# Kernel optimization log

Hardware: AMD Instinct MI355X
Metric: run time of the kernel (lower is better)

The kernel has to match this reference:

```python
import jax, jax.numpy as jnp
import numpy as np
from jax import lax

WIN = 11
SIGMA = 1.5
C1 = 0.01 ** 2
C2 = 0.03 ** 2


def _gauss_window(c):
    x = np.arange(WIN) - WIN // 2
    g = np.exp(-(x ** 2) / (2.0 * SIGMA ** 2))
    g = g / g.sum()
    w2d = np.outer(g, g).astype(np.float32)  # [11,11]
    return jnp.asarray(np.broadcast_to(w2d, (c, 1, WIN, WIN)).copy())


def _dwconv(x, kernel, groups):
    # x: [B,C,H,W], kernel: [C,1,kh,kw] depthwise, stride 1, SAME padding
    return lax.conv_general_dilated(
        x, kernel, window_strides=(1, 1), padding='SAME',
        dimension_numbers=('NCHW', 'OIHW', 'NCHW'),
        feature_group_count=groups)


_SOBEL_X = jnp.asarray(np.array([[-1, 0, 1], [-2, 0, 2], [-1, 0, 1]], np.float32))
_SOBEL_Y = jnp.asarray(np.array([[1, 2, 1], [0, 0, 0], [-1, -2, -1]], np.float32))


def _sobel_xy(x):
    # x: [B,3,H,W] -> depthwise 3x3 sobel on each channel (same as per-channel conv2d)
    c = x.shape[1]
    kx = jnp.broadcast_to(_SOBEL_X, (c, 1, 3, 3))
    ky = jnp.broadcast_to(_SOBEL_Y, (c, 1, 3, 3))
    return _dwconv(x, kx, c), _dwconv(x, ky, c)


def _rgb2ycrcb(im):
    R, G, B = im[:, 0:1], im[:, 1:2], im[:, 2:3]
    Y = 0.299 * R + 0.587 * G + 0.114 * B
    Cr = (R - Y) * 0.713 + 0.5
    Cb = (B - Y) * 0.564 + 0.5
    return Y, Cr, Cb


def _ssim(img1, img2, channel):
    w = _gauss_window(channel)
    mu1 = _dwconv(img1, w, channel)
    mu2 = _dwconv(img2, w, channel)
    mu1_sq = mu1 * mu1
    mu2_sq = mu2 * mu2
    mu12 = mu1 * mu2
    s1 = _dwconv(img1 * img1, w, channel) - mu1_sq
    s2 = _dwconv(img2 * img2, w, channel) - mu2_sq
    s12 = _dwconv(img1 * img2, w, channel) - mu12
    ssim_map = ((2 * mu12 + C1) * (2 * s12 + C2)) / ((mu1_sq + mu2_sq + C1) * (s1 + s2 + C2))
    return ssim_map.mean()


def _l1(a, b):
    return jnp.mean(jnp.abs(a - b))


def setup_inputs() -> dict:
    key = jax.random.key(0)
    k1, k2, k3 = jax.random.split(key, 3)
    shp = (16, 3, 512, 512)
    return {
        'input_vis': jax.random.uniform(k1, shp, jnp.float32),
        'input_ir': jax.random.uniform(k2, shp, jnp.float32),
        'fuse': jax.random.uniform(k3, shp, jnp.float32),
    }


def reference(input_vis, input_ir, fuse):
    # color components
    _, Cr_F, Cb_F = _rgb2ycrcb(fuse)
    _, Cr_V, Cb_V = _rgb2ycrcb(input_vis)
    Y_ir = input_ir[:, 0:1]

    # sobel gradients (depthwise over 3 channels == per-channel conv + cat)
    Fgx, Fgy = _sobel_xy(fuse)
    Vgx, Vgy = _sobel_xy(input_vis)
    Igx, Igy = _sobel_xy(input_ir)
    joint_gx = jnp.maximum(Vgx, Igx)
    joint_gy = jnp.maximum(Vgy, Igy)
    joint_int = jnp.maximum(input_vis, input_ir)

    con_loss = _l1(fuse, joint_int)
    gradient_loss = 0.5 * _l1(Fgx, joint_gx) + 0.5 * _l1(Fgy, joint_gy)
    color_loss = _l1(Cb_F, Cb_V) + _l1(Cr_F, Cr_V)

    # SSIM: rgb-vs-fused (3ch) and ir-Y vs gray(fused) (1ch)
    ssim_rgb = _ssim(input_vis, fuse, 3)
    gray_fused = (0.2989 * fuse[:, 0:1] + 0.587 * fuse[:, 1:2] + 0.114 * fuse[:, 2:3])
    ssim_ir = _ssim(Y_ir, gray_fused, 1)
    ssim_loss = 1.0 - (ssim_rgb + ssim_ir) / 2.0

    return 0.5 * con_loss + 0.2 * gradient_loss + 1.0 * color_loss + 0.1 * ssim_loss
```

## Files before the change

kernel.cpp:

```cpp
#include <hip/hip_runtime.h>

#define IMG_H 512
#define IMG_W 512
#define CH_STRIDE (IMG_H*IMG_W)
#define IMG_STRIDE (3*CH_STRIDE)

using f4 = __attribute__((ext_vector_type(4))) float;
using h2 = __attribute__((ext_vector_type(2))) _Float16;
using h4 = __attribute__((ext_vector_type(4))) _Float16;
using h8 = __attribute__((ext_vector_type(8))) _Float16;

#define NSLOT 64
#define SLOT_F 32

__global__ __launch_bounds__(256) void k_zero(float* __restrict__ acc) {
  int i = threadIdx.x;
  *(f4*)&acc[i*8]     = f4{0,0,0,0};
  *(f4*)&acc[i*8 + 4] = f4{0,0,0,0};
}

__device__ __forceinline__ float block_sum(float v, float* red) {
  #pragma unroll
  for (int o = 32; o > 0; o >>= 1) v += __shfl_down(v, o, 64);
  __syncthreads();
  if ((threadIdx.x & 63) == 0) red[threadIdx.x >> 6] = v;
  __syncthreads();
  return red[0] + red[1] + red[2] + red[3];
}

__device__ __forceinline__ h8 splat8(_Float16 v) { return h8{v,v,v,v,v,v,v,v}; }

#define R1W 68
#define R1N (18*R1W)

#define SXW 80
#define SXH 42
#define HB8 264
#define SSIM_SX_B (SXH*SXW*2)
#define SSIM_HB_B (SXH*HB8*2)
#define SMEM_BYTES (2*SSIM_SX_B + SSIM_HB_B)

__global__ __launch_bounds__(256, 4) void k_main(
    const float* __restrict__ vis, const float* __restrict__ ir,
    const float* __restrict__ fuse, float* __restrict__ acc)
{
  __shared__ __align__(16) char smem[SMEM_BYTES];
  __shared__ float red[4];
  const int tid = threadIdx.x;
  const int bid = blockIdx.x;
  float* aslot = acc + (bid & (NSLOT-1))*SLOT_F;

  if (bid < 8192) {
    const int z = bid >> 7;
    const int n = z >> 2, pair = z & 3;
    const int x0 = (bid & 7)*64;
    const int y0 = ((bid >> 3) & 15)*32;
    _Float16* sx = (_Float16*)smem;
    _Float16* sy = (_Float16*)(smem + SSIM_SX_B);
    _Float16* hb = (_Float16*)(smem + 2*SSIM_SX_B);

    _Float16 gh[11];
    h2 gh2[11];
    {
      const float gu[6] = {0.00386592014f, 0.02856550078f, 0.13533528324f,
                           0.41111229050f, 0.80073740292f, 1.0f};
      float g[11], gs = 0.f;
      #pragma unroll
      for (int i = 0; i < 11; ++i) { g[i] = gu[i < 6 ? i : 10 - i]; gs += g[i]; }
      #pragma unroll
      for (int i = 0; i < 11; ++i) {
        g[i] /= gs;
        gh[i] = (_Float16)g[i];
        gh2[i] = h2{gh[i], gh[i]};
      }
    }

    if (pair < 3) {
      const float* xb = vis  + (n*3 + pair)*CH_STRIDE;
      const float* yb = fuse + (n*3 + pair)*CH_STRIDE;
      for (int i = tid; i < SXH*20; i += 256) {
        int row = i / 20, k = i - row*20;
        int gy = y0 - 5 + row, gx = x0 - 8 + 4*k;
        f4 xv = {0,0,0,0}, yv = {0,0,0,0};
        if ((unsigned)gy < IMG_H && (unsigned)gx < IMG_W) {
          int off = gy*IMG_W + gx;
          xv = *(const f4*)&xb[off];
          yv = *(const f4*)&yb[off];
        }
        int ib = row*SXW + 4*k;
        *(h4*)&sx[ib] = h4{(_Float16)xv.x,(_Float16)xv.y,(_Float16)xv.z,(_Float16)xv.w};
        *(h4*)&sy[ib] = h4{(_Float16)yv.x,(_Float16)yv.y,(_Float16)yv.z,(_Float16)yv.w};
      }
    } else {
      const float* xb = ir   + n*IMG_STRIDE;
      const float* fb = fuse + n*IMG_STRIDE;
      for (int i = tid; i < SXH*20; i += 256) {
        int row = i / 20, k = i - row*20;
        int gy = y0 - 5 + row, gx = x0 - 8 + 4*k;
        f4 xv = {0,0,0,0}, yv = {0,0,0,0};
        if ((unsigned)gy < IMG_H && (unsigned)gx < IMG_W) {
          int off = gy*IMG_W + gx;
          xv = *(const f4*)&xb[off];
          f4 rr = *(const f4*)&fb[off];
          f4 gg = *(const f4*)&fb[off + CH_STRIDE];
          f4 bb = *(const f4*)&fb[off + 2*CH_STRIDE];
          #pragma unroll
          for (int j = 0; j < 4; ++j)
            yv[j] = 0.2989f*rr[j] + 0.587f*gg[j] + 0.114f*bb[j];
        }
        int ib = row*SXW + 4*k;
        *(h4*)&sx[ib] = h4{(_Float16)xv.x,(_Float16)xv.y,(_Float16)xv.z,(_Float16)xv.w};
        *(h4*)&sy[ib] = h4{(_Float16)yv.x,(_Float16)yv.y,(_Float16)yv.z,(_Float16)yv.w};
      }
    }
    __syncthreads();

    for (int t = tid; t < SXH*8; t += 256) {
      int row = t >> 3, p0 = (t & 7)*4;
      int base = row*SXW + p0*2;
      h8 xa0 = *(const h8*)&sx[base];
      h8 xa1 = *(const h8*)&sx[base+8];
      h8 xa2 = *(const h8*)&sx[base+16];
      h8 yb0 = *(const h8*)&sy[base];
      h8 yb1 = *(const h8*)&sy[base+8];
      h8 yb2 = *(const h8*)&sy[base+16];
      _Float16 wa[21], wb[21];
      #pragma unroll
      for (int u = 0; u < 21; ++u) {
        wa[u] = (u < 8 ? xa0[u] : (u < 16 ? xa1[u-8] : xa2[u-16]));
        wb[u] = (u < 8 ? yb0[u] : (u < 16 ? yb1[u-8] : yb2[u-16]));
      }
      h2 pa[14], pb[14], pp[14], pq[14];
      #pragma unroll
      for (int u = 0; u < 14; ++u) {
        pa[u] = h2{wa[u+3], wa[u+7]};
        pb[u] = h2{wb[u+3], wb[u+7]};
        pp[u] = pa[u]*pa[u] + pb[u]*pb[u];
        pq[u] = pa[u]*pb[u];
      }
      h2 cA[4], cB[4], cP[4], cQ[4];
      #pragma unroll
      for (int j = 0; j < 4; ++j) { cA[j]=h2{0,0}; cB[j]=h2{0,0}; cP[j]=h2{0,0}; cQ[j]=h2{0,0}; }
      #pragma unroll
      for (int k = 0; k < 11; ++k) {
        h2 gk = gh2[k];
        #pragma unroll
        for (int j = 0; j < 4; ++j) {
          cA[j] += gk * pa[k+j];
          cB[j] += gk * pb[k+j];
          cP[j] += gk * pp[k+j];
          cQ[j] += gk * pq[k+j];
        }
      }
      #pragma unroll
      for (int p = 0; p < 4; ++p) {
        int j0 = 2*p, j1 = 2*p + 1;
        _Float16 a0 = (j0 < 4) ? cA[j0][0] : cA[j0-4][1];
        _Float16 b0 = (j0 < 4) ? cB[j0][0] : cB[j0-4][1];
        _Float16 P0 = (j0 < 4) ? cP[j0][0] : cP[j0-4][1];
        _Float16 q0 = (j0 < 4) ? cQ[j0][0] : cQ[j0-4][1];
        _Float16 a1 = (j1 < 4) ? cA[j1][0] : cA[j1-4][1];
        _Float16 b1 = (j1 < 4) ? cB[j1][0] : cB[j1-4][1];
        _Float16 P1 = (j1 < 4) ? cP[j1][0] : cP[j1-4][1];
        _Float16 q1 = (j1 < 4) ? cQ[j1][0] : cQ[j1-4][1];
        *(h8*)&hb[row*HB8 + (p0 + p)*8] = h8{a0,b0,P0,q0,a1,b1,P1,q1};
      }
    }
    __syncthreads();

    const int xp = tid & 31;
    const int ybase = (tid >> 5)*4;
    h8 vacc[4];
    #pragma unroll
    for (int m = 0; m < 4; ++m) vacc[m] = splat8((_Float16)0.f);
    #pragma unroll
    for (int r = 0; r < 14; ++r) {
      h8 rv = *(const h8*)&hb[(ybase + r)*HB8 + xp*8];
      #pragma unroll
      for (int m = 0; m < 4; ++m) {
        int k = r - m;
        if (k >= 0 && k < 11) vacc[m] += splat8(gh[k]) * rv;
      }
    }

    float ss = 0.f;
    #pragma unroll
    for (int m = 0; m < 4; ++m) {
      #pragma unroll
      for (int px = 0; px < 2; ++px) {
        float mu1 = (float)vacc[m][4*px + 0];
        float mu2 = (float)vacc[m][4*px + 1];
        float sP  = (float)vacc[m][4*px + 2];
        float sQ  = (float)vacc[m][4*px + 3];
        float mu12 = mu1*mu2, mss = mu1*mu1 + mu2*mu2;
        float s12 = sQ - mu12, sps = sP - mss;
        ss += ((2.f*mu12 + 1e-4f)*(2.f*s12 + 9e-4f)) /
              ((mss + 1e-4f)*(sps + 9e-4f));
      }
    }
    float tot = block_sum(ss, red);
    if (tid == 0) atomicAdd(&aslot[(pair == 3) ? 6 : 5], tot);

  } else {
    const int r = bid - 8192;
    const int x0 = (r & 7)*64;
    const int y0 = ((r >> 3) & 31)*16;
    const int n  = r >> 8;
    float* s = (float*)smem;
    const int ox = (tid & 15)*4;
    const int oy = tid >> 4;

    float con=0.f, gxs=0.f, gys=0.f, cbs=0.f, crs=0.f;
    float pv[3][4], pf[3][4];

    for (int c = 0; c < 3; ++c) {
      const float* pv0 = vis  + (n*3 + c)*CH_STRIDE;
      const float* pi0 = ir   + (n*3 + c)*CH_STRIDE;
      const float* pf0 = fuse + (n*3 + c)*CH_STRIDE;
      for (int i = tid; i < 864; i += 256) {
        int f = i / 288;
        int rr = i - f*288;
        int row = rr >> 4, k = rr & 15;
        int gy = y0 - 1 + row, gx = x0 + 4*k;
        f4 v = {0,0,0,0};
        const float* bp = (f == 0) ? pv0 : ((f == 1) ? pi0 : pf0);
        if ((unsigned)gy < IMG_H) v = *(const f4*)&bp[gy*IMG_W + gx];
        float* dst = s + f*R1N + row*R1W + 1 + 4*k;
        dst[0]=v.x; dst[1]=v.y; dst[2]=v.z; dst[3]=v.w;
      }
      if (tid < 108) {
        int f = tid / 36;
        int rr = tid - f*36;
        int row = rr >> 1, side = rr & 1;
        int gy = y0 - 1 + row;
        int gx = side ? (x0 + 64) : (x0 - 1);
        float v = 0.f;
        const float* bp = (f == 0) ? pv0 : ((f == 1) ? pi0 : pf0);
        if ((unsigned)gx < IMG_W && (unsigned)gy < IMG_H) v = bp[gy*IMG_W + gx];
        s[f*R1N + row*R1W + (side ? 65 : 0)] = v;
      }
      __syncthreads();

      float cen[3][4], gxv[3][4], gyv[3][4];
      #pragma unroll
      for (int t = 0; t < 3; ++t) {
        const float* sf = s + t*R1N;
        float r0[8], r1[8], r2[8];
        {
          f4 a = *(const f4*)&sf[(oy+0)*R1W + ox], b = *(const f4*)&sf[(oy+0)*R1W + ox + 4];
          r0[0]=a.x; r0[1]=a.y; r0[2]=a.z; r0[3]=a.w; r0[4]=b.x; r0[5]=b.y; r0[6]=b.z; r0[7]=b.w;
        }
        {
          f4 a = *(const f4*)&sf[(oy+1)*R1W + ox], b = *(const f4*)&sf[(oy+1)*R1W + ox + 4];
          r1[0]=a.x; r1[1]=a.y; r1[2]=a.z; r1[3]=a.w; r1[4]=b.x; r1[5]=b.y; r1[6]=b.z; r1[7]=b.w;
        }
        {
          f4 a = *(const f4*)&sf[(oy+2)*R1W + ox], b = *(const f4*)&sf[(oy+2)*R1W + ox + 4];
          r2[0]=a.x; r2[1]=a.y; r2[2]=a.z; r2[3]=a.w; r2[4]=b.x; r2[5]=b.y; r2[6]=b.z; r2[7]=b.w;
        }
        #pragma unroll
        for (int j = 0; j < 4; ++j) {
          gxv[t][j] = (r0[j+2]-r0[j]) + 2.f*(r1[j+2]-r1[j]) + (r2[j+2]-r2[j]);
          gyv[t][j] = (r0[j] + 2.f*r0[j+1] + r0[j+2]) - (r2[j] + 2.f*r2[j+1] + r2[j+2]);
          cen[t][j] = r1[j+1];
        }
      }
      #pragma unroll
      for (int j = 0; j < 4; ++j) {
        con += fabsf(cen[2][j] - fmaxf(cen[0][j], cen[1][j]));
        gxs += fabsf(gxv[2][j] - fmaxf(gxv[0][j], gxv[1][j]));
        gys += fabsf(gyv[2][j] - fmaxf(gyv[0][j], gyv[1][j]));
        pv[c][j] = cen[0][j];
        pf[c][j] = cen[2][j];
      }
      __syncthreads();
    }

    #pragma unroll
    for (int j = 0; j < 4; ++j) {
      float Yf = 0.299f*pf[0][j] + 0.587f*pf[1][j] + 0.114f*pf[2][j];
      float Yv = 0.299f*pv[0][j] + 0.587f*pv[1][j] + 0.114f*pv[2][j];
      crs += fabsf(0.713f*((pf[0][j]-Yf) - (pv[0][j]-Yv)));
      cbs += fabsf(0.564f*((pf[2][j]-Yf) - (pv[2][j]-Yv)));
    }

    float r0 = block_sum(con, red);
    float r1 = block_sum(gxs, red);
    float r2 = block_sum(gys, red);
    float r3 = block_sum(cbs, red);
    float r4 = block_sum(crs, red);
    if (tid == 0) {
      atomicAdd(&aslot[0], r0);
      atomicAdd(&aslot[1], r1);
      atomicAdd(&aslot[2], r2);
      atomicAdd(&aslot[3], r3);
      atomicAdd(&aslot[4], r4);
    }
  }
}

__global__ __launch_bounds__(64) void k_final(
    const float* __restrict__ acc, float* __restrict__ out)
{
  int lane = threadIdx.x;
  float s[7];
  #pragma unroll
  for (int c = 0; c < 7; ++c) {
    float x = acc[lane*SLOT_F + c];
    #pragma unroll
    for (int o = 32; o > 0; o >>= 1) x += __shfl_down(x, o, 64);
    s[c] = x;
  }
  if (lane == 0) {
    const float N3 = 16.f*3.f*512.f*512.f;
    const float N1 = 16.f*512.f*512.f;
    float con_loss  = s[0] / N3;
    float grad_loss = 0.5f*(s[1]/N3) + 0.5f*(s[2]/N3);
    float color_loss = s[3]/N1 + s[4]/N1;
    float ssim_loss = 1.f - (s[5]/N3 + s[6]/N1)*0.5f;
    out[0] = 0.5f*con_loss + 0.2f*grad_loss + color_loss + 0.1f*ssim_loss;
  }
}

extern "C" void kernel_launch(void* const* d_in, const int* in_sizes, int n_in,
                              void* d_out, int out_size, void* d_ws, size_t ws_size,
                              hipStream_t stream) {
  (void)in_sizes; (void)n_in; (void)out_size; (void)ws_size;
  const float* vis  = (const float*)d_in[0];
  const float* ir   = (const float*)d_in[1];
  const float* fuse = (const float*)d_in[2];
  float* out = (float*)d_out;
  float* acc = (float*)d_ws;

  k_zero<<<dim3(1,1,1), dim3(256,1,1), 0, stream>>>(acc);
  k_main<<<dim3(12288,1,1), dim3(256,1,1), 0, stream>>>(vis, ir, fuse, acc);
  k_final<<<dim3(1,1,1), dim3(64,1,1), 0, stream>>>(acc, out);
}
```

Baseline: 245.4 us.

## Pack adjacent pixels into half2 lanes and remap block order across XCDs

The horizontal Gaussian pass now pairs adjacent pixels (even/odd phase) in each half2 instead of pixels four apart. This removes the lane-shuffling extracts when packing results into shared memory, and the packed hb layout changes to planar per-quantity pairs, so the vertical pass indexing is updated to match. Block IDs are also remapped so that consecutive hardware blocks, which are spread round-robin across the 8 XCDs, map to contiguous work ranges per XCD, aiming for better L2 locality. The remap assumes the grid size is 8*1536 blocks; any other grid size would break the mapping.

```diff
diff --git a/kernel.cpp b/kernel.cpp
--- a/kernel.cpp
+++ b/kernel.cpp
@@ -48,13 +48,14 @@
   __shared__ float red[4];
   const int tid = threadIdx.x;
   const int bid = blockIdx.x;
+  const int sbid = (bid & 7)*1536 + (bid >> 3);
   float* aslot = acc + (bid & (NSLOT-1))*SLOT_F;
 
-  if (bid < 8192) {
-    const int z = bid >> 7;
+  if (sbid < 8192) {
+    const int z = sbid >> 7;
     const int n = z >> 2, pair = z & 3;
-    const int x0 = (bid & 7)*64;
-    const int y0 = ((bid >> 3) & 15)*32;
+    const int x0 = (sbid & 7)*64;
+    const int y0 = ((sbid >> 3) & 15)*32;
     _Float16* sx = (_Float16*)smem;
     _Float16* sy = (_Float16*)(smem + SSIM_SX_B);
     _Float16* hb = (_Float16*)(smem + 2*SSIM_SX_B);
@@ -124,46 +125,56 @@
       h8 yb0 = *(const h8*)&sy[base];
       h8 yb1 = *(const h8*)&sy[base+8];
       h8 yb2 = *(const h8*)&sy[base+16];
-      _Float16 wa[21], wb[21];
-      #pragma unroll
-      for (int u = 0; u < 21; ++u) {
-        wa[u] = (u < 8 ? xa0[u] : (u < 16 ? xa1[u-8] : xa2[u-16]));
-        wb[u] = (u < 8 ? yb0[u] : (u < 16 ? yb1[u-8] : yb2[u-16]));
-      }
-      h2 pa[14], pb[14], pp[14], pq[14];
-      #pragma unroll
-      for (int u = 0; u < 14; ++u) {
-        pa[u] = h2{wa[u+3], wa[u+7]};
-        pb[u] = h2{wb[u+3], wb[u+7]};
-        pp[u] = pa[u]*pa[u] + pb[u]*pb[u];
-        pq[u] = pa[u]*pb[u];
+      _Float16 wa[24], wb[24];
+      #pragma unroll
+      for (int u = 0; u < 8; ++u) {
+        wa[u] = xa0[u]; wa[u+8] = xa1[u]; wa[u+16] = xa2[u];
+        wb[u] = yb0[u]; wb[u+8] = yb1[u]; wb[u+16] = yb2[u];
+      }
+      h2 WA[10], WB[10], WP[10], WQ[10];
+      #pragma unroll
+      for (int m = 2; m < 10; ++m) {
+        WA[m] = h2{wa[2*m], wa[2*m+1]};
+        WB[m] = h2{wb[2*m], wb[2*m+1]};
+        WP[m] = WA[m]*WA[m] + WB[m]*WB[m];
+        WQ[m] = WA[m]*WB[m];
+      }
+      h2 WAo[10], WBo[10], WPo[10], WQo[10];
+      #pragma unroll
+      for (int m = 1; m < 10; ++m) {
+        WAo[m] = h2{wa[2*m+1], wa[2*m+2]};
+        WBo[m] = h2{wb[2*m+1], wb[2*m+2]};
+        WPo[m] = WAo[m]*WAo[m] + WBo[m]*WBo[m];
+        WQo[m] = WAo[m]*WBo[m];
       }
       h2 cA[4], cB[4], cP[4], cQ[4];
       #pragma unroll
-      for (int j = 0; j < 4; ++j) { cA[j]=h2{0,0}; cB[j]=h2{0,0}; cP[j]=h2{0,0}; cQ[j]=h2{0,0}; }
+      for (int p = 0; p < 4; ++p) { cA[p]=h2{0,0}; cB[p]=h2{0,0}; cP[p]=h2{0,0}; cQ[p]=h2{0,0}; }
       #pragma unroll
       for (int k = 0; k < 11; ++k) {
         h2 gk = gh2[k];
         #pragma unroll
-        for (int j = 0; j < 4; ++j) {
-          cA[j] += gk * pa[k+j];
-          cB[j] += gk * pb[k+j];
-          cP[j] += gk * pp[k+j];
-          cQ[j] += gk * pq[k+j];
+        for (int p = 0; p < 4; ++p) {
+          int o = k + 3 + 2*p;
+          int m = o >> 1;
+          if (o & 1) {
+            cA[p] += gk * WAo[m];
+            cB[p] += gk * WBo[m];
+            cP[p] += gk * WPo[m];
+            cQ[p] += gk * WQo[m];
+          } else {
+            cA[p] += gk * WA[m];
+            cB[p] += gk * WB[m];
+            cP[p] += gk * WP[m];
+            cQ[p] += gk * WQ[m];
+          }
         }
       }
       #pragma unroll
       for (int p = 0; p < 4; ++p) {
-        int j0 = 2*p, j1 = 2*p + 1;
-        _Float16 a0 = (j0 < 4) ? cA[j0][0] : cA[j0-4][1];
-        _Float16 b0 = (j0 < 4) ? cB[j0][0] : cB[j0-4][1];
-        _Float16 P0 = (j0 < 4) ? cP[j0][0] : cP[j0-4][1];
-        _Float16 q0 = (j0 < 4) ? cQ[j0][0] : cQ[j0-4][1];
-        _Float16 a1 = (j1 < 4) ? cA[j1][0] : cA[j1-4][1];
-        _Float16 b1 = (j1 < 4) ? cB[j1][0] : cB[j1-4][1];
-        _Float16 P1 = (j1 < 4) ? cP[j1][0] : cP[j1-4][1];
-        _Float16 q1 = (j1 < 4) ? cQ[j1][0] : cQ[j1-4][1];
-        *(h8*)&hb[row*HB8 + (p0 + p)*8] = h8{a0,b0,P0,q0,a1,b1,P1,q1};
+        *(h8*)&hb[row*HB8 + (p0 + p)*8] =
+            h8{cA[p][0], cA[p][1], cB[p][0], cB[p][1],
+               cP[p][0], cP[p][1], cQ[p][0], cQ[p][1]};
       }
     }
     __syncthreads();
@@ -188,10 +199,10 @@
     for (int m = 0; m < 4; ++m) {
       #pragma unroll
       for (int px = 0; px < 2; ++px) {
-        float mu1 = (float)vacc[m][4*px + 0];
-        float mu2 = (float)vacc[m][4*px + 1];
-        float sP  = (float)vacc[m][4*px + 2];
-        float sQ  = (float)vacc[m][4*px + 3];
+        float mu1 = (float)vacc[m][0 + px];
+        float mu2 = (float)vacc[m][2 + px];
+        float sP  = (float)vacc[m][4 + px];
+        float sQ  = (float)vacc[m][6 + px];
         float mu12 = mu1*mu2, mss = mu1*mu1 + mu2*mu2;
         float s12 = sQ - mu12, sps = sP - mss;
         ss += ((2.f*mu12 + 1e-4f)*(2.f*s12 + 9e-4f)) /
@@ -202,7 +213,7 @@
     if (tid == 0) atomicAdd(&aslot[(pair == 3) ? 6 : 5], tot);
 
   } else {
-    const int r = bid - 8192;
+    const int r = sbid - 8192;
     const int x0 = (r & 7)*64;
     const int y0 = ((r >> 3) & 31)*16;
     const int n  = r >> 8;
```

After: 270.6 us. 1.1x slower.
